# Kernel optimization log

Hardware: AMD Instinct MI355X
Metric: run time of the kernel (lower is better)

## Reference

```python
import jax, jax.numpy as jnp
import numpy as np

DIM = 1024
NUM_HEADS = 16
HEAD_DIM = DIM // NUM_HEADS
WINDOW = 128
EPS = 1e-5


def setup_inputs() -> dict:
    key = jax.random.key(0)
    ks = jax.random.split(key, 8)
    B, S, D = 1, 2048, DIM
    x = jax.random.normal(ks[0], (B, S, D), dtype=jnp.float32)
    # xavier-uniform-ish scale for linear weights (torch layout: [out, in])
    def xavier(k, out_f, in_f):
        lim = np.sqrt(6.0 / (in_f + out_f)).astype(np.float32)
        return jax.random.uniform(k, (out_f, in_f), jnp.float32, -lim, lim)
    qkv_w = xavier(ks[1], 3 * D, D)
    out_w = xavier(ks[2], D, D)
    ln_g = jnp.ones((D,), jnp.float32)
    ln_b = jnp.zeros((D,), jnp.float32)
    w1 = xavier(ks[3], 4 * D, D)
    b1 = jnp.zeros((4 * D,), jnp.float32)
    w2 = xavier(ks[4], D, 4 * D)
    b2 = jnp.zeros((D,), jnp.float32)
    return {"x": x, "qkv_w": qkv_w, "out_w": out_w, "ln_g": ln_g,
            "ln_b": ln_b, "w1": w1, "b1": b1, "w2": w2, "b2": b2}


def reference(x, qkv_w, out_w, ln_g, ln_b, w1, b1, w2, b2):
    B, S, D = x.shape
    H, hd = NUM_HEADS, HEAD_DIM
    residual = x
    # LayerNorm (pre-norm)
    mu = jnp.mean(x, axis=-1, keepdims=True)
    var = jnp.var(x, axis=-1, keepdims=True)
    xn = (x - mu) * jax.lax.rsqrt(var + EPS) * ln_g + ln_b
    # QKV projection (torch Linear: y = x @ W^T)
    qkv = xn @ qkv_w.T                              # [B,S,3D]
    qkv = qkv.reshape(B, S, 3, H, hd).transpose(2, 0, 3, 1, 4)  # [3,B,H,S,hd]
    q, k, v = qkv[0], qkv[1], qkv[2]
    # Local-window boolean mask: |i - j| <= window_size // 2
    w = WINDOW // 2
    i = jnp.arange(S)[:, None]
    j = jnp.arange(S)[None, :]
    local_mask = jnp.abs(i - j) <= w                # [S,S]
    # SDPA with boolean mask
    scale = 1.0 / np.sqrt(hd).astype(np.float32)
    scores = jnp.einsum('bhqd,bhkd->bhqk', q, k) * scale
    scores = jnp.where(local_mask, scores, -jnp.inf)
    attn = jax.nn.softmax(scores, axis=-1)
    attn_out = jnp.einsum('bhqk,bhkd->bhqd', attn, v)
    attn_out = attn_out.transpose(0, 2, 1, 3).reshape(B, S, D)
    attn_out = attn_out @ out_w.T
    out = residual + attn_out
    # FFN (no second norm in this module), exact GELU
    h = jax.nn.gelu(out @ w1.T + b1, approximate=False)
    ffn_out = h @ w2.T + b2
    return out + ffn_out
```

## Files before the change

kernel.cpp:

```cpp
#include <hip/hip_runtime.h>
#include <math.h>

typedef unsigned short u16;
typedef __attribute__((ext_vector_type(8))) short short8;
typedef __attribute__((ext_vector_type(4))) float f32x4;
typedef __attribute__((ext_vector_type(4))) int i32x4;

__device__ inline u16 f2bf(float f){
  union { float f; unsigned int u; } x; x.f = f;
  unsigned int r = x.u + 0x7fffu + ((x.u >> 16) & 1u);
  return (u16)(r >> 16);
}

__global__ __launch_bounds__(256) void cvt_bf16(const float* __restrict__ in, u16* __restrict__ out, int n){
  int i = (blockIdx.x * 256 + threadIdx.x) * 4;
  if (i + 3 < n){
    float4 v = *(const float4*)(in + i);
    out[i]   = f2bf(v.x);
    out[i+1] = f2bf(v.y);
    out[i+2] = f2bf(v.z);
    out[i+3] = f2bf(v.w);
  }
}

__global__ __launch_bounds__(256) void ln_kernel(const float* __restrict__ x, const float* __restrict__ g,
                                                 const float* __restrict__ b, u16* __restrict__ xn){
  const int row = blockIdx.x;
  const int tid = threadIdx.x;
  float4 v = *(const float4*)(x + (size_t)row*1024 + tid*4);
  float s  = v.x + v.y + v.z + v.w;
  float ss = v.x*v.x + v.y*v.y + v.z*v.z + v.w*v.w;
  #pragma unroll
  for (int off = 32; off; off >>= 1){
    s  += __shfl_xor(s,  off, 64);
    ss += __shfl_xor(ss, off, 64);
  }
  __shared__ float red[8];
  const int wid = tid >> 6;
  if ((tid & 63) == 0){ red[wid] = s; red[4+wid] = ss; }
  __syncthreads();
  float S  = red[0]+red[1]+red[2]+red[3];
  float SS = red[4]+red[5]+red[6]+red[7];
  float mu  = S * (1.0f/1024.0f);
  float var = SS * (1.0f/1024.0f) - mu*mu;
  float rs  = rsqrtf(var + 1e-5f);
  float4 gv = *(const float4*)(g + tid*4);
  float4 bv = *(const float4*)(b + tid*4);
  size_t o = (size_t)row*1024 + tid*4;
  xn[o]   = f2bf((v.x-mu)*rs*gv.x + bv.x);
  xn[o+1] = f2bf((v.y-mu)*rs*gv.y + bv.y);
  xn[o+2] = f2bf((v.z-mu)*rs*gv.z + bv.z);
  xn[o+3] = f2bf((v.w-mu)*rs*gv.w + bv.w);
}

template<int EPI>
__global__ __launch_bounds__(256) void gemm_lds(
    const u16* __restrict__ A, const u16* __restrict__ B,
    float* __restrict__ outF, u16* __restrict__ outB,
    const float* __restrict__ bias, const float* __restrict__ resid,
    int M, int N, int K, int nbx, int nwg, int Kc)
{
  __shared__ u16 As[128*64];
  __shared__ u16 Bs[64*64];
  const int tid = threadIdx.x;
  const int l   = tid & 63;
  const int w   = tid >> 6;
  const int wr  = w >> 1, wc = w & 1;
  const int orig = blockIdx.x;
  const int wgid = (orig & 7) * (nwg >> 3) + (orig >> 3);
  const int bcol = wgid % nbx, brow = wgid / nbx;
  const int kz = blockIdx.y;
  const int l15 = l & 15, l4 = l >> 4;

  const u16* Ab = A + (size_t)brow*128*K + (size_t)kz*Kc;
  const u16* Bb = B + (size_t)bcol*64*K  + (size_t)kz*Kc;

  f32x4 acc[4][2];
  #pragma unroll
  for (int i = 0; i < 4; ++i)
    #pragma unroll
    for (int j = 0; j < 2; ++j)
      acc[i][j] = (f32x4){0.f, 0.f, 0.f, 0.f};

  const int rsub = l >> 3;
  const int csrc = ((l & 7) ^ rsub) * 8;
  const int swz  = (l15 & 7) * 8;
  const int nkt = Kc >> 6;
  for (int kt = 0; kt < nkt; ++kt){
    const u16* Ag = Ab + kt*64 + csrc;
    const u16* Bg = Bb + kt*64 + csrc;
    #pragma unroll
    for (int i = 0; i < 4; ++i){
      const int ca = w*4 + i;
      __builtin_amdgcn_global_load_lds(
        (const __attribute__((address_space(1))) void*)(Ag + (size_t)(ca*8 + rsub)*K),
        (__attribute__((address_space(3))) void*)(As + ca*512), 16, 0, 0);
    }
    #pragma unroll
    for (int i = 0; i < 2; ++i){
      const int cb = w*2 + i;
      __builtin_amdgcn_global_load_lds(
        (const __attribute__((address_space(1))) void*)(Bg + (size_t)(cb*8 + rsub)*K),
        (__attribute__((address_space(3))) void*)(Bs + cb*512), 16, 0, 0);
    }
    __syncthreads();
    #pragma unroll
    for (int ks = 0; ks < 2; ++ks){
      const int kop = (ks*32 + l4*8) ^ swz;
      short8 af[4], bfr[2];
      #pragma unroll
      for (int i = 0; i < 4; ++i) af[i]  = *(const short8*)&As[(wr*64 + i*16 + l15)*64 + kop];
      #pragma unroll
      for (int j = 0; j < 2; ++j) bfr[j] = *(const short8*)&Bs[(wc*32 + j*16 + l15)*64 + kop];
      #pragma unroll
      for (int i = 0; i < 4; ++i)
        #pragma unroll
        for (int j = 0; j < 2; ++j)
          acc[i][j] = __builtin_amdgcn_mfma_f32_16x16x32_bf16(af[i], bfr[j], acc[i][j], 0, 0, 0);
    }
    __syncthreads();
  }

  #pragma unroll
  for (int i = 0; i < 4; ++i){
    #pragma unroll
    for (int j = 0; j < 2; ++j){
      #pragma unroll
      for (int r = 0; r < 4; ++r){
        int row = brow*128 + wr*64 + i*16 + l4*4 + r;
        int col = bcol*64 + wc*32 + j*16 + l15;
        float v = acc[i][j][r];
        size_t o = (size_t)row * N + col;
        if constexpr (EPI == 0){
          outB[o] = f2bf(v);
        } else if constexpr (EPI == 1){
          v += resid[o];
          outF[o] = v;
          outB[o] = f2bf(v);
        } else if constexpr (EPI == 2){
          v += bias[col];
          v = 0.5f * v * (1.0f + erff(v * 0.70710678118654752f));
          outB[o] = f2bf(v);
        } else {
          outF[(size_t)kz * M * N + o] = v;
        }
      }
    }
  }
}

__global__ __launch_bounds__(256) void reduce_ffn2(const float* __restrict__ p,
                                                   const float* __restrict__ bias,
                                                   const float* __restrict__ resid,
                                                   float* __restrict__ out){
  const size_t s = (size_t)2048*1024;
  const size_t i = ((size_t)blockIdx.x * 256 + threadIdx.x) * 4;
  float4 a0 = *(const float4*)(p + i);
  float4 a1 = *(const float4*)(p + s + i);
  float4 a2 = *(const float4*)(p + 2*s + i);
  float4 a3 = *(const float4*)(p + 3*s + i);
  float4 r  = *(const float4*)(resid + i);
  float4 bb = *(const float4*)(bias + (i & 1023));
  float4 o;
  o.x = a0.x + a1.x + a2.x + a3.x + r.x + bb.x;
  o.y = a0.y + a1.y + a2.y + a3.y + r.y + bb.y;
  o.z = a0.z + a1.z + a2.z + a3.z + r.z + bb.z;
  o.w = a0.w + a1.w + a2.w + a3.w + r.w + bb.w;
  *(float4*)(out + i) = o;
}

__global__ __launch_bounds__(256) void attn_kernel(const u16* __restrict__ qkv, u16* __restrict__ attn_out){
  constexpr int S = 2048, D3 = 3072;
  const int qt = blockIdx.x, h = blockIdx.y;
  const int q0 = qt * 64;
  const int tid = threadIdx.x;
  const int l = tid & 63, w = tid >> 6;
  const int l15 = l & 15, l4 = l >> 4;

  __shared__ u16 smem[31232];
  u16 (*Qs)[72]  = (u16(*)[72]) (smem);
  u16 (*Ks)[72]  = (u16(*)[72]) (smem + 4608);
  u16 (*Ps)[200] = (u16(*)[200])(smem + 4608);
  u16 (*Vt)[200] = (u16(*)[200])(smem + 18432);

  #pragma unroll
  for (int i = 0; i < 2; ++i){
    int cid = tid + 256*i; int r = cid >> 3, c = cid & 7;
    *(i32x4*)&Qs[r][c*8] = *(const i32x4*)(qkv + (size_t)(q0 + r)*D3 + h*64 + c*8);
  }
  #pragma unroll
  for (int i = 0; i < 6; ++i){
    int cid = tid + 256*i; int r = cid >> 3, c = cid & 7;
    int kj = q0 - 64 + r;
    i32x4 kv = {0,0,0,0}, vv = {0,0,0,0};
    if (kj >= 0 && kj < S){
      kv = *(const i32x4*)(qkv + (size_t)kj*D3 + 1024 + h*64 + c*8);
      vv = *(const i32x4*)(qkv + (size_t)kj*D3 + 2048 + h*64 + c*8);
    }
    *(i32x4*)&Ks[r][c*8] = kv;
    union { i32x4 v; u16 u[8]; } uu; uu.v = vv;
    #pragma unroll
    for (int j = 0; j < 8; ++j) Vt[c*8 + j][r] = uu.u[j];
  }
  __syncthreads();

  f32x4 sc[12];
  #pragma unroll
  for (int cf = 0; cf < 12; ++cf) sc[cf] = (f32x4){0.f,0.f,0.f,0.f};
  const int ko = l4 * 8;
  short8 a0 = *(const short8*)&Qs[16*w + l15][ko];
  short8 a1 = *(const short8*)&Qs[16*w + l15][32 + ko];
  #pragma unroll
  for (int cf = 0; cf < 12; ++cf){
    short8 b0 = *(const short8*)&Ks[cf*16 + l15][ko];
    short8 b1 = *(const short8*)&Ks[cf*16 + l15][32 + ko];
    sc[cf] = __builtin_amdgcn_mfma_f32_16x16x32_bf16(a0, b0, sc[cf], 0, 0, 0);
    sc[cf] = __builtin_amdgcn_mfma_f32_16x16x32_bf16(a1, b1, sc[cf], 0, 0, 0);
  }
  __syncthreads();

  const float scale = 0.125f;
  #pragma unroll
  for (int r = 0; r < 4; ++r){
    const int qrl = 16*w + l4*4 + r;
    float mx = -1e30f;
    #pragma unroll
    for (int cf = 0; cf < 12; ++cf){
      int j  = cf*16 + l15;
      int kj = q0 - 64 + j;
      bool ok = (j >= qrl) && (j <= qrl + 128) && (kj >= 0) && (kj < S);
      float sv = ok ? sc[cf][r]*scale : -1e30f;
      sc[cf][r] = sv;
      mx = fmaxf(mx, sv);
    }
    #pragma unroll
    for (int off = 1; off < 16; off <<= 1) mx = fmaxf(mx, __shfl_xor(mx, off, 64));
    float sm = 0.f;
    #pragma unroll
    for (int cf = 0; cf < 12; ++cf){
      float pv = __expf(sc[cf][r] - mx);
      sc[cf][r] = pv;
      sm += pv;
    }
    #pragma unroll
    for (int off = 1; off < 16; off <<= 1) sm += __shfl_xor(sm, off, 64);
    float inv = 1.0f / sm;
    #pragma unroll
    for (int cf = 0; cf < 12; ++cf) Ps[qrl][cf*16 + l15] = f2bf(sc[cf][r] * inv);
  }
  __syncthreads();

  f32x4 o[4];
  #pragma unroll
  for (int df = 0; df < 4; ++df) o[df] = (f32x4){0.f,0.f,0.f,0.f};
  #pragma unroll
  for (int kk = 0; kk < 6; ++kk){
    short8 a = *(const short8*)&Ps[16*w + l15][kk*32 + ko];
    #pragma unroll
    for (int df = 0; df < 4; ++df){
      short8 b = *(const short8*)&Vt[df*16 + l15][kk*32 + ko];
      o[df] = __builtin_amdgcn_mfma_f32_16x16x32_bf16(a, b, o[df], 0, 0, 0);
    }
  }
  #pragma unroll
  for (int df = 0; df < 4; ++df){
    #pragma unroll
    for (int r = 0; r < 4; ++r){
      attn_out[(size_t)(q0 + 16*w + l4*4 + r)*1024 + h*64 + df*16 + l15] = f2bf(o[df][r]);
    }
  }
}

extern "C" void kernel_launch(void* const* d_in, const int* in_sizes, int n_in,
                              void* d_out, int out_size, void* d_ws, size_t ws_size,
                              hipStream_t stream)
{
  const float* x     = (const float*)d_in[0];
  const float* qkv_w = (const float*)d_in[1];
  const float* out_w = (const float*)d_in[2];
  const float* ln_g  = (const float*)d_in[3];
  const float* ln_b  = (const float*)d_in[4];
  const float* w1    = (const float*)d_in[5];
  const float* b1    = (const float*)d_in[6];
  const float* w2    = (const float*)d_in[7];
  const float* b2    = (const float*)d_in[8];
  float* out_final = (float*)d_out;

  char* p = (char*)d_ws;
  u16* xn_b   = (u16*)p; p += (size_t)2048*1024*2;
  u16* qkv_b  = (u16*)p; p += (size_t)2048*3072*2;
  u16* attn_b = (u16*)p; p += (size_t)2048*1024*2;
  u16* out_b  = (u16*)p; p += (size_t)2048*1024*2;
  u16* qkvw_b = (u16*)p; p += (size_t)3072*1024*2;
  u16* outw_b = (u16*)p; p += (size_t)1024*1024*2;
  u16* w1_b   = (u16*)p; p += (size_t)4096*1024*2;
  u16* w2_b   = (u16*)p; p += (size_t)1024*4096*2;
  float* out_f= (float*)p; p += (size_t)2048*1024*4;
  u16* h_b    = (u16*)p; p += (size_t)2048*4096*2;

  float* partials = (float*)xn_b;

  cvt_bf16<<<3072, 256, 0, stream>>>(qkv_w, qkvw_b, 3072*1024);
  cvt_bf16<<<1024, 256, 0, stream>>>(out_w, outw_b, 1024*1024);
  cvt_bf16<<<4096, 256, 0, stream>>>(w1,    w1_b,   4096*1024);
  cvt_bf16<<<4096, 256, 0, stream>>>(w2,    w2_b,   1024*4096);
  ln_kernel<<<2048, 256, 0, stream>>>(x, ln_g, ln_b, xn_b);
  gemm_lds<0><<<dim3(768), 256, 0, stream>>>(xn_b, qkvw_b, nullptr, qkv_b, nullptr, nullptr,
                                             2048, 3072, 1024, 48, 768, 1024);
  attn_kernel<<<dim3(32,16), 256, 0, stream>>>(qkv_b, attn_b);
  gemm_lds<1><<<dim3(256), 256, 0, stream>>>(attn_b, outw_b, out_f, out_b, nullptr, x,
                                             2048, 1024, 1024, 16, 256, 1024);
  gemm_lds<2><<<dim3(1024), 256, 0, stream>>>(out_b, w1_b, nullptr, h_b, b1, nullptr,
                                              2048, 4096, 1024, 64, 1024, 1024);
  gemm_lds<4><<<dim3(256, 4), 256, 0, stream>>>(h_b, w2_b, partials, nullptr, nullptr, nullptr,
                                                2048, 1024, 4096, 16, 256, 1024);
  reduce_ffn2<<<2048, 256, 0, stream>>>(partials, b2, out_f, out_final);
}
```

Baseline: 139.5 us.

## Fuse prep kernels, double-buffer GEMM LDS, and use 2-wave 64x64 warp tiles

The four weight-conversion launches and the LayerNorm launch become a single prep kernel that writes packed 4-element bf16 stores. The GEMM moves to 128 threads, with each wave computing a 64x64 sub-tile (4x4 MFMA accumulators) instead of 64x32. LDS is double-buffered so the next K tile is issued before the current one is computed. This cuts launch overhead and improves register-level reuse and load/compute overlap. In exchange it uses twice the LDS and more registers per thread, and halving the thread count may lower occupancy.

```diff
diff --git a/kernel.cpp b/kernel.cpp
--- a/kernel.cpp
+++ b/kernel.cpp
@@ -5,6 +5,7 @@
 typedef __attribute__((ext_vector_type(8))) short short8;
 typedef __attribute__((ext_vector_type(4))) float f32x4;
 typedef __attribute__((ext_vector_type(4))) int i32x4;
+typedef __attribute__((ext_vector_type(4))) u16 u16x4;
 
 __device__ inline u16 f2bf(float f){
   union { float f; unsigned int u; } x; x.f = f;
@@ -12,60 +13,70 @@
   return (u16)(r >> 16);
 }
 
-__global__ __launch_bounds__(256) void cvt_bf16(const float* __restrict__ in, u16* __restrict__ out, int n){
-  int i = (blockIdx.x * 256 + threadIdx.x) * 4;
-  if (i + 3 < n){
-    float4 v = *(const float4*)(in + i);
-    out[i]   = f2bf(v.x);
-    out[i+1] = f2bf(v.y);
-    out[i+2] = f2bf(v.z);
-    out[i+3] = f2bf(v.w);
-  }
-}
-
-__global__ __launch_bounds__(256) void ln_kernel(const float* __restrict__ x, const float* __restrict__ g,
-                                                 const float* __restrict__ b, u16* __restrict__ xn){
-  const int row = blockIdx.x;
+__global__ __launch_bounds__(256) void prep_kernel(
+    const float* __restrict__ x, const float* __restrict__ g, const float* __restrict__ b,
+    u16* __restrict__ xn,
+    const float* __restrict__ qkv_w, u16* __restrict__ qkvw_b,
+    const float* __restrict__ out_w, u16* __restrict__ outw_b,
+    const float* __restrict__ w1,    u16* __restrict__ w1_b,
+    const float* __restrict__ w2,    u16* __restrict__ w2_b)
+{
   const int tid = threadIdx.x;
-  float4 v = *(const float4*)(x + (size_t)row*1024 + tid*4);
-  float s  = v.x + v.y + v.z + v.w;
-  float ss = v.x*v.x + v.y*v.y + v.z*v.z + v.w*v.w;
-  #pragma unroll
-  for (int off = 32; off; off >>= 1){
-    s  += __shfl_xor(s,  off, 64);
-    ss += __shfl_xor(ss, off, 64);
-  }
-  __shared__ float red[8];
-  const int wid = tid >> 6;
-  if ((tid & 63) == 0){ red[wid] = s; red[4+wid] = ss; }
-  __syncthreads();
-  float S  = red[0]+red[1]+red[2]+red[3];
-  float SS = red[4]+red[5]+red[6]+red[7];
-  float mu  = S * (1.0f/1024.0f);
-  float var = SS * (1.0f/1024.0f) - mu*mu;
-  float rs  = rsqrtf(var + 1e-5f);
-  float4 gv = *(const float4*)(g + tid*4);
-  float4 bv = *(const float4*)(b + tid*4);
-  size_t o = (size_t)row*1024 + tid*4;
-  xn[o]   = f2bf((v.x-mu)*rs*gv.x + bv.x);
-  xn[o+1] = f2bf((v.y-mu)*rs*gv.y + bv.y);
-  xn[o+2] = f2bf((v.z-mu)*rs*gv.z + bv.z);
-  xn[o+3] = f2bf((v.w-mu)*rs*gv.w + bv.w);
+  int bid = blockIdx.x;
+  if (bid < 2048){
+    const int row = bid;
+    float4 v = *(const float4*)(x + (size_t)row*1024 + tid*4);
+    float s  = v.x + v.y + v.z + v.w;
+    float ss = v.x*v.x + v.y*v.y + v.z*v.z + v.w*v.w;
+    #pragma unroll
+    for (int off = 32; off; off >>= 1){
+      s  += __shfl_xor(s,  off, 64);
+      ss += __shfl_xor(ss, off, 64);
+    }
+    __shared__ float red[8];
+    const int wid = tid >> 6;
+    if ((tid & 63) == 0){ red[wid] = s; red[4+wid] = ss; }
+    __syncthreads();
+    float S  = red[0]+red[1]+red[2]+red[3];
+    float SS = red[4]+red[5]+red[6]+red[7];
+    float mu  = S * (1.0f/1024.0f);
+    float var = SS * (1.0f/1024.0f) - mu*mu;
+    float rs  = rsqrtf(var + 1e-5f);
+    float4 gv = *(const float4*)(g + tid*4);
+    float4 bv = *(const float4*)(b + tid*4);
+    u16x4 pk;
+    pk.x = f2bf((v.x-mu)*rs*gv.x + bv.x);
+    pk.y = f2bf((v.y-mu)*rs*gv.y + bv.y);
+    pk.z = f2bf((v.z-mu)*rs*gv.z + bv.z);
+    pk.w = f2bf((v.w-mu)*rs*gv.w + bv.w);
+    *(u16x4*)(xn + (size_t)row*1024 + tid*4) = pk;
+    return;
+  }
+  bid -= 2048;
+  const float* src; u16* dst;
+  if (bid < 3072){ src = qkv_w; dst = qkvw_b; }
+  else if (bid < 3072+1024){ src = out_w; dst = outw_b; bid -= 3072; }
+  else if (bid < 3072+1024+4096){ src = w1; dst = w1_b; bid -= 3072+1024; }
+  else { src = w2; dst = w2_b; bid -= 3072+1024+4096; }
+  const size_t i = ((size_t)bid*256 + tid) * 4;
+  float4 v = *(const float4*)(src + i);
+  u16x4 pk;
+  pk.x = f2bf(v.x); pk.y = f2bf(v.y); pk.z = f2bf(v.z); pk.w = f2bf(v.w);
+  *(u16x4*)(dst + i) = pk;
 }
 
 template<int EPI>
-__global__ __launch_bounds__(256) void gemm_lds(
+__global__ __launch_bounds__(128) void gemm_lds(
     const u16* __restrict__ A, const u16* __restrict__ B,
     float* __restrict__ outF, u16* __restrict__ outB,
     const float* __restrict__ bias, const float* __restrict__ resid,
     int M, int N, int K, int nbx, int nwg, int Kc)
 {
-  __shared__ u16 As[128*64];
-  __shared__ u16 Bs[64*64];
+  __shared__ u16 As[2][128*64];
+  __shared__ u16 Bs[2][64*64];
   const int tid = threadIdx.x;
   const int l   = tid & 63;
   const int w   = tid >> 6;
-  const int wr  = w >> 1, wc = w & 1;
   const int orig = blockIdx.x;
   const int wgid = (orig & 7) * (nwg >> 3) + (orig >> 3);
   const int bcol = wgid % nbx, brow = wgid / nbx;
@@ -75,47 +86,54 @@
   const u16* Ab = A + (size_t)brow*128*K + (size_t)kz*Kc;
   const u16* Bb = B + (size_t)bcol*64*K  + (size_t)kz*Kc;
 
-  f32x4 acc[4][2];
+  f32x4 acc[4][4];
   #pragma unroll
   for (int i = 0; i < 4; ++i)
     #pragma unroll
-    for (int j = 0; j < 2; ++j)
+    for (int j = 0; j < 4; ++j)
       acc[i][j] = (f32x4){0.f, 0.f, 0.f, 0.f};
 
   const int rsub = l >> 3;
   const int csrc = ((l & 7) ^ rsub) * 8;
   const int swz  = (l15 & 7) * 8;
   const int nkt = Kc >> 6;
-  for (int kt = 0; kt < nkt; ++kt){
+
+  auto stage = [&](int kt, int buf){
     const u16* Ag = Ab + kt*64 + csrc;
     const u16* Bg = Bb + kt*64 + csrc;
     #pragma unroll
-    for (int i = 0; i < 4; ++i){
-      const int ca = w*4 + i;
+    for (int i = 0; i < 8; ++i){
+      const int ca = w*8 + i;
       __builtin_amdgcn_global_load_lds(
         (const __attribute__((address_space(1))) void*)(Ag + (size_t)(ca*8 + rsub)*K),
-        (__attribute__((address_space(3))) void*)(As + ca*512), 16, 0, 0);
-    }
-    #pragma unroll
-    for (int i = 0; i < 2; ++i){
-      const int cb = w*2 + i;
+        (__attribute__((address_space(3))) void*)(&As[buf][ca*512]), 16, 0, 0);
+    }
+    #pragma unroll
+    for (int i = 0; i < 4; ++i){
+      const int cb = w*4 + i;
       __builtin_amdgcn_global_load_lds(
         (const __attribute__((address_space(1))) void*)(Bg + (size_t)(cb*8 + rsub)*K),
-        (__attribute__((address_space(3))) void*)(Bs + cb*512), 16, 0, 0);
-    }
-    __syncthreads();
+        (__attribute__((address_space(3))) void*)(&Bs[buf][cb*512]), 16, 0, 0);
+    }
+  };
+
+  stage(0, 0);
+  __syncthreads();
+  for (int kt = 0; kt < nkt; ++kt){
+    const int cur = kt & 1;
+    if (kt + 1 < nkt) stage(kt + 1, cur ^ 1);
     #pragma unroll
     for (int ks = 0; ks < 2; ++ks){
       const int kop = (ks*32 + l4*8) ^ swz;
-      short8 af[4], bfr[2];
+      short8 af[4], bfr[4];
       #pragma unroll
-      for (int i = 0; i < 4; ++i) af[i]  = *(const short8*)&As[(wr*64 + i*16 + l15)*64 + kop];
+      for (int i = 0; i < 4; ++i) af[i]  = *(const short8*)&As[cur][(w*64 + i*16 + l15)*64 + kop];
       #pragma unroll
-      for (int j = 0; j < 2; ++j) bfr[j] = *(const short8*)&Bs[(wc*32 + j*16 + l15)*64 + kop];
+      for (int j = 0; j < 4; ++j) bfr[j] = *(const short8*)&Bs[cur][(j*16 + l15)*64 + kop];
       #pragma unroll
       for (int i = 0; i < 4; ++i)
         #pragma unroll
-        for (int j = 0; j < 2; ++j)
+        for (int j = 0; j < 4; ++j)
           acc[i][j] = __builtin_amdgcn_mfma_f32_16x16x32_bf16(af[i], bfr[j], acc[i][j], 0, 0, 0);
     }
     __syncthreads();
@@ -124,11 +142,11 @@
   #pragma unroll
   for (int i = 0; i < 4; ++i){
     #pragma unroll
-    for (int j = 0; j < 2; ++j){
+    for (int j = 0; j < 4; ++j){
       #pragma unroll
       for (int r = 0; r < 4; ++r){
-        int row = brow*128 + wr*64 + i*16 + l4*4 + r;
-        int col = bcol*64 + wc*32 + j*16 + l15;
+        int row = brow*128 + w*64 + i*16 + l4*4 + r;
+        int col = bcol*64 + j*16 + l15;
         float v = acc[i][j][r];
         size_t o = (size_t)row * N + col;
         if constexpr (EPI == 0){
@@ -300,19 +318,17 @@
 
   float* partials = (float*)xn_b;
 
-  cvt_bf16<<<3072, 256, 0, stream>>>(qkv_w, qkvw_b, 3072*1024);
-  cvt_bf16<<<1024, 256, 0, stream>>>(out_w, outw_b, 1024*1024);
-  cvt_bf16<<<4096, 256, 0, stream>>>(w1,    w1_b,   4096*1024);
-  cvt_bf16<<<4096, 256, 0, stream>>>(w2,    w2_b,   1024*4096);
-  ln_kernel<<<2048, 256, 0, stream>>>(x, ln_g, ln_b, xn_b);
-  gemm_lds<0><<<dim3(768), 256, 0, stream>>>(xn_b, qkvw_b, nullptr, qkv_b, nullptr, nullptr,
+  prep_kernel<<<14336, 256, 0, stream>>>(x, ln_g, ln_b, xn_b,
+                                         qkv_w, qkvw_b, out_w, outw_b,
+                                         w1, w1_b, w2, w2_b);
+  gemm_lds<0><<<dim3(768), 128, 0, stream>>>(xn_b, qkvw_b, nullptr, qkv_b, nullptr, nullptr,
                                              2048, 3072, 1024, 48, 768, 1024);
   attn_kernel<<<dim3(32,16), 256, 0, stream>>>(qkv_b, attn_b);
-  gemm_lds<1><<<dim3(256), 256, 0, stream>>>(attn_b, outw_b, out_f, out_b, nullptr, x,
+  gemm_lds<1><<<dim3(256), 128, 0, stream>>>(attn_b, outw_b, out_f, out_b, nullptr, x,
                                              2048, 1024, 1024, 16, 256, 1024);
-  gemm_lds<2><<<dim3(1024), 256, 0, stream>>>(out_b, w1_b, nullptr, h_b, b1, nullptr,
+  gemm_lds<2><<<dim3(1024), 128, 0, stream>>>(out_b, w1_b, nullptr, h_b, b1, nullptr,
                                               2048, 4096, 1024, 64, 1024, 1024);
-  gemm_lds<4><<<dim3(256, 4), 256, 0, stream>>>(h_b, w2_b, partials, nullptr, nullptr, nullptr,
+  gemm_lds<4><<<dim3(256, 4), 128, 0, stream>>>(h_b, w2_b, partials, nullptr, nullptr, nullptr,
                                                 2048, 1024, 4096, 16, 256, 1024);
   reduce_ffn2<<<2048, 256, 0, stream>>>(partials, b2, out_f, out_final);
 }
```

Result: slower. 165.2 us (+18.5%).
